# Optimization experiments

Measured on AMD Instinct MI355X. Metric: run time of the kernel, lower is better.

## Reference

```python
import jax, jax.numpy as jnp
import numpy as np

D = 1024
H = 16
HD = D // H
S = 2048
B = 4
EPS = 1e-5


def gelu_tanh(x):
    c = jnp.sqrt(2.0 / jnp.pi).astype(x.dtype)
    return 0.5 * x * (1.0 + jnp.tanh(c * (x + 0.044715 * x ** 3)))


def layernorm(x, gamma, beta):
    mu = jnp.mean(x, axis=-1, keepdims=True)
    var = jnp.var(x, axis=-1, keepdims=True)
    return (x - mu) * jax.lax.rsqrt(var + EPS) * gamma + beta


def setup_inputs() -> dict:
    key = jax.random.key(0)
    ks = jax.random.split(key, 12)
    s = 0.02
    return {
        "x": jax.random.normal(ks[0], (B, S, D), jnp.float32),
        "Wq": jax.random.normal(ks[1], (D, D), jnp.float32) * s,
        "Wk": jax.random.normal(ks[2], (D, D), jnp.float32) * s,
        "Wv": jax.random.normal(ks[3], (D, D), jnp.float32) * s,
        "Wo": jax.random.normal(ks[4], (D, D), jnp.float32) * s,
        "bo": jnp.zeros((D,), jnp.float32),
        "W1": jax.random.normal(ks[5], (D, 4 * D), jnp.float32) * s,
        "b1": jnp.zeros((4 * D,), jnp.float32),
        "W2": jax.random.normal(ks[6], (4 * D, D), jnp.float32) * s,
        "b2": jnp.zeros((D,), jnp.float32),
        "g1": jnp.ones((D,), jnp.float32),
        "be1": jnp.zeros((D,), jnp.float32),
        "g2": jnp.ones((D,), jnp.float32),
        "be2": jnp.zeros((D,), jnp.float32),
    }


def reference(x, Wq, Wk, Wv, Wo, bo, W1, b1, W2, b2, g1, be1, g2, be2):
    b, n, d = x.shape
    # --- attention sub-block (pre-LN) ---
    h = layernorm(x, g1, be1)
    q = (h @ Wq).reshape(b, n, H, HD).transpose(0, 2, 1, 3)  # [b,H,n,hd]
    k = (h @ Wk).reshape(b, n, H, HD).transpose(0, 2, 1, 3)
    v = (h @ Wv).reshape(b, n, H, HD).transpose(0, 2, 1, 3)
    scores = jnp.einsum('bhqd,bhkd->bhqk', q, k) / jnp.sqrt(jnp.float32(HD))
    causal = jnp.tril(jnp.ones((n, n), dtype=bool))
    scores = jnp.where(causal, scores, -jnp.inf)
    w = jax.nn.softmax(scores, axis=-1)  # dropout rate 0 -> identity
    attn = jnp.einsum('bhqk,bhkd->bhqd', w, v)
    attn = attn.transpose(0, 2, 1, 3).reshape(b, n, d)
    x = x + (attn @ Wo + bo)
    # --- FFN sub-block (pre-LN) ---
    h = layernorm(x, g2, be2)
    h = gelu_tanh(h @ W1 + b1) @ W2 + b2
    return x + h
```

## Files before the change

### kernel.cpp

```cpp
#include <hip/hip_runtime.h>
#include <hip/hip_bf16.h>
#include <math.h>


typedef __attribute__((ext_vector_type(8))) short bf16x8;
typedef __attribute__((ext_vector_type(4))) float f32x4;

#define AS1 __attribute__((address_space(1)))
#define AS3 __attribute__((address_space(3)))

__device__ __forceinline__ void gl_lds16(const void* g, void* l) {
  __builtin_amdgcn_global_load_lds((const AS1 void*)g, (AS3 void*)l, 16, 0, 0);
}

__device__ __forceinline__ float gelu_f(float x) {
  const float c = 0.7978845608028654f;
  return 0.5f * x * (1.0f + tanhf(c * (x + 0.044715f * x * x * x)));
}

__device__ __forceinline__ float bf2f(short s) {
  unsigned u = ((unsigned)(unsigned short)s) << 16;
  return __builtin_bit_cast(float, u);
}
__device__ __forceinline__ short f2bf(float f) {
  __hip_bfloat16 h = __float2bfloat16(f);
  return __builtin_bit_cast(short, h);
}

__global__ void __launch_bounds__(256) tcvt_kernel(
    const float* __restrict__ W, __hip_bfloat16* __restrict__ WT, int K, int N) {
  __shared__ float t[32][33];
  const int n0 = blockIdx.x * 32, k0 = blockIdx.y * 32;
  const int tx = threadIdx.x, ty0 = threadIdx.y;
#pragma unroll
  for (int i = 0; i < 4; i++) {
    int ty = ty0 + i * 8;
    t[ty][tx] = W[(size_t)(k0 + ty) * N + n0 + tx];
  }
  __syncthreads();
#pragma unroll
  for (int i = 0; i < 4; i++) {
    int ty = ty0 + i * 8;
    WT[(size_t)(n0 + ty) * K + k0 + tx] = __float2bfloat16(t[tx][ty]);
  }
}

__global__ void __launch_bounds__(256) vtr_kernel(
    const __hip_bfloat16* __restrict__ qkv, __hip_bfloat16* __restrict__ vt) {
  __shared__ __hip_bfloat16 t[32][33];
  const int s0 = blockIdx.x * 32;
  const int hd0 = blockIdx.y * 32;
  const int bh = blockIdx.z;
  const int b = bh >> 4, h = bh & 15;
  const int tx = threadIdx.x, ty0 = threadIdx.y;
  const __hip_bfloat16* src =
      qkv + (size_t)(b * 2048 + s0) * 3072 + 2048 + h * 64 + hd0;
#pragma unroll
  for (int i = 0; i < 4; i++) {
    int ty = ty0 + i * 8;
    t[ty][tx] = src[(size_t)ty * 3072 + tx];
  }
  __syncthreads();
  __hip_bfloat16* dst = vt + ((size_t)bh * 64 + hd0) * 2048 + s0;
#pragma unroll
  for (int i = 0; i < 4; i++) {
    int ty = ty0 + i * 8;
    dst[(size_t)ty * 2048 + tx] = t[tx][ty];
  }
}

__global__ void __launch_bounds__(256) ln_kernel(
    const float* __restrict__ x, const float* __restrict__ gma,
    const float* __restrict__ bta, __hip_bfloat16* __restrict__ out) {
  const int row = blockIdx.x;
  const int tid = threadIdx.x;
  const float4 v = ((const float4*)(x + (size_t)row * 1024))[tid];
  float s = v.x + v.y + v.z + v.w;
  float s2 = v.x * v.x + v.y * v.y + v.z * v.z + v.w * v.w;
#pragma unroll
  for (int m = 32; m; m >>= 1) {
    s += __shfl_xor(s, m);
    s2 += __shfl_xor(s2, m);
  }
  __shared__ float red[8];
  const int w = tid >> 6, lane = tid & 63;
  if (lane == 0) { red[w] = s; red[4 + w] = s2; }
  __syncthreads();
  s = red[0] + red[1] + red[2] + red[3];
  s2 = red[4] + red[5] + red[6] + red[7];
  const float mu = s * (1.0f / 1024.0f);
  const float var = s2 * (1.0f / 1024.0f) - mu * mu;
  const float rs = rsqrtf(var + 1e-5f);
  const float4 gv = ((const float4*)gma)[tid];
  const float4 bv = ((const float4*)bta)[tid];
  __hip_bfloat16* orow = out + (size_t)row * 1024 + tid * 4;
  orow[0] = __float2bfloat16((v.x - mu) * rs * gv.x + bv.x);
  orow[1] = __float2bfloat16((v.y - mu) * rs * gv.y + bv.y);
  orow[2] = __float2bfloat16((v.z - mu) * rs * gv.z + bv.z);
  orow[3] = __float2bfloat16((v.w - mu) * rs * gv.w + bv.w);
}

template <int BM, int BN, int WM, int WN, int EPI>
__global__ void __launch_bounds__(512, 2) gemmT(
    const __hip_bfloat16* __restrict__ Ap, const __hip_bfloat16* __restrict__ Bp,
    void* __restrict__ outp, const float* __restrict__ bias,
    const float* __restrict__ resid, int N, int K) {
  constexpr int PM = BM / WM, PN = BN / WN;
  constexpr int MR = PM / 16, NR = PN / 16;
  constexpr int UA = BM / 128, UB = BN / 128, U = UA + UB;
  constexpr int KSB = (BM + BN) * 64;
  __shared__ __attribute__((aligned(128))) char smem[2 * 2 * KSB];
  const int tid = threadIdx.x;
  const int lane = tid & 63, w = tid >> 6;
  const int wr = w / WN, wc = w % WN;
  const int cr = lane & 15, g = lane >> 4;

  const int gx = gridDim.x;
  const int nwg = gx * gridDim.y;
  const int orig = blockIdx.y * gx + blockIdx.x;
  const int f = (orig & 7) * (nwg >> 3) + (orig >> 3);
  const int sid = f >> 4, wit = f & 15;
  const int stm = gx >> 2;
  const int bm = (sid % stm) * 4 + (wit & 3);
  const int bn = (sid / stm) * 4 + (wit >> 2);
  const int bmr = bm * BM, bnr = bn * BN;
  const int nkt = K >> 6;

  const int srow = tid >> 2;
  const int sq = ((tid & 3) ^ (((srow >> 3) & 1) << 1)) * 8;
  const int rq = (g ^ (((cr >> 3) & 1) << 1)) * 8;

  auto stage_ks = [&](int tt, int ks) {
    char* base = smem + (tt & 1) * (2 * KSB) + ks * KSB;
#pragma unroll
    for (int ua = 0; ua < UA; ua++)
      gl_lds16(Ap + (size_t)(bmr + ua * 128 + srow) * K + tt * 64 + ks * 32 + sq,
               base + ua * 8192 + w * 1024);
#pragma unroll
    for (int ub = 0; ub < UB; ub++)
      gl_lds16(Bp + (size_t)(bnr + ub * 128 + srow) * K + tt * 64 + ks * 32 + sq,
               base + BM * 64 + ub * 8192 + w * 1024);
  };
  auto vmw = [&]() {
    if constexpr (U == 3)
      asm volatile("s_waitcnt vmcnt(9)" ::: "memory");
    else
      asm volatile("s_waitcnt vmcnt(12)" ::: "memory");
  };

  f32x4 acc[MR][NR];
#pragma unroll
  for (int i = 0; i < MR; i++)
#pragma unroll
    for (int j = 0; j < NR; j++) acc[i][j] = (f32x4){0.f, 0.f, 0.f, 0.f};

  auto compute = [&](int t, int ks) {
    const char* base = smem + (t & 1) * (2 * KSB) + ks * KSB;
    const __hip_bfloat16* pA = (const __hip_bfloat16*)base;
    const __hip_bfloat16* pB = (const __hip_bfloat16*)(base + BM * 64);
    bf16x8 av[MR], bv[NR];
#pragma unroll
    for (int m = 0; m < MR; m++)
      av[m] = *(const bf16x8*)(pA + (wr * PM + m * 16 + cr) * 32 + rq);
#pragma unroll
    for (int n = 0; n < NR; n++)
      bv[n] = *(const bf16x8*)(pB + (wc * PN + n * 16 + cr) * 32 + rq);
    __builtin_amdgcn_s_setprio(1);
#pragma unroll
    for (int m = 0; m < MR; m++)
#pragma unroll
      for (int n = 0; n < NR; n++)
        acc[m][n] =
            __builtin_amdgcn_mfma_f32_16x16x32_bf16(av[m], bv[n], acc[m][n], 0, 0, 0);
    __builtin_amdgcn_s_setprio(0);
  };

  stage_ks(0, 0);
  stage_ks(0, 1);
  stage_ks(1, 0);

  for (int t = 0; t < nkt; ++t) {
    stage_ks(t + 1 < nkt ? t + 1 : t - 1, 1);
    vmw();
    __builtin_amdgcn_s_barrier();
    compute(t, 0);
    __builtin_amdgcn_s_barrier();
    stage_ks(t + 2 < nkt ? t + 2 : t, 0);
    vmw();
    __builtin_amdgcn_s_barrier();
    compute(t, 1);
    __builtin_amdgcn_s_barrier();
  }
  asm volatile("s_waitcnt vmcnt(0)" ::: "memory");

#pragma unroll
  for (int m = 0; m < MR; m++) {
#pragma unroll
    for (int rr = 0; rr < 4; rr++) {
      const int row = bmr + wr * PM + m * 16 + g * 4 + rr;
#pragma unroll
      for (int n = 0; n < NR; n++) {
        const int col = bnr + wc * PN + n * 16 + cr;
        float v = acc[m][n][rr];
        if (EPI == 0) {
          ((__hip_bfloat16*)outp)[(size_t)row * N + col] = __float2bfloat16(v);
        } else if (EPI == 1) {
          v += bias[col] + resid[(size_t)row * N + col];
          ((float*)outp)[(size_t)row * N + col] = v;
        } else {
          v = gelu_f(v + bias[col]);
          ((__hip_bfloat16*)outp)[(size_t)row * N + col] = __float2bfloat16(v);
        }
      }
    }
  }
}

__global__ void __launch_bounds__(256) attn_kernel(
    const __hip_bfloat16* __restrict__ qkv, const __hip_bfloat16* __restrict__ vt,
    __hip_bfloat16* __restrict__ o) {
  __shared__ __hip_bfloat16 sK[2][64 * 64];
  __shared__ __hip_bfloat16 sV[2][64 * 64];
  __shared__ __hip_bfloat16 pl[4][16][64];
  const int tid = threadIdx.x, lane = tid & 63, w = tid >> 6;
  const int bid = blockIdx.x;
  const int bh = (bid & 7) + 8 * ((bid >> 3) & 7);
  const int qt = 15 - (bid >> 6);
  const int b = bh >> 4, h = bh & 15;
  const int cr = lane & 15, g = lane >> 4;
  const int qr0 = qt * 128 + w * 32;
  const float NEG = -1e30f;
  const float SC2 = 0.18033688011112042f;
  const int sw = cr & 7;
  const int sg0 = (g ^ sw) * 8;
  const int sg1 = ((g ^ sw) ^ 4) * 8;
  const int pkey = (cr & 7) << 1;

  bf16x8 aq[2][2];
#pragma unroll
  for (int m = 0; m < 2; m++) {
    const __hip_bfloat16* qp =
        qkv + (size_t)(b * 2048 + qr0 + m * 16 + cr) * 3072 + h * 64 + g * 8;
    bf16x8 q0 = *(const bf16x8*)qp;
    bf16x8 q1 = *(const bf16x8*)(qp + 32);
#pragma unroll
    for (int j = 0; j < 8; j++) {
      aq[m][0][j] = f2bf(bf2f(q0[j]) * SC2);
      aq[m][1][j] = f2bf(bf2f(q1[j]) * SC2);
    }
  }
  const __hip_bfloat16* kbase = qkv + (size_t)(b * 2048) * 3072 + 1024 + h * 64;
  const __hip_bfloat16* vbase = vt + (size_t)bh * 64 * 2048;

  const int l8 = lane >> 3, c8 = lane & 7;
  const int c8s = (c8 ^ l8) * 8;
#define STAGE_TILE(bi, ktile)                                                   \
  {                                                                             \
    _Pragma("unroll") for (int i = 0; i < 2; i++) {                             \
      const int rb = (i * 4 + w) * 8 + l8;                                      \
      gl_lds16(kbase + (size_t)((ktile) * 64 + rb) * 3072 + c8s,                \
               &sK[bi][(i * 4 + w) * 512]);                                     \
      gl_lds16(vbase + (size_t)rb * 2048 + (ktile) * 64 + c8s,                  \
               &sV[bi][(i * 4 + w) * 512]);                                     \
    }                                                                           \
  }

  f32x4 oacc[2][4];
#pragma unroll
  for (int m = 0; m < 2; m++)
#pragma unroll
    for (int i = 0; i < 4; i++) oacc[m][i] = (f32x4){0.f, 0.f, 0.f, 0.f};
  float mrow[2] = {NEG, NEG};
  float lrow[2] = {0.f, 0.f};

  const int nkt = (qt + 1) * 2;
  STAGE_TILE(0, 0);
  asm volatile("s_waitcnt vmcnt(0)" ::: "memory");
  __syncthreads();
  int cur = 0;

  for (int kt = 0; kt < nkt; ++kt) {
    if (kt + 1 < nkt) STAGE_TILE(cur ^ 1, kt + 1);

    if (kt * 64 <= qr0 + 31) {
      f32x4 st[4][2];
      __builtin_amdgcn_s_setprio(1);
#pragma unroll
      for (int kf = 0; kf < 4; kf++) {
        const bf16x8 bk0 = *(const bf16x8*)&sK[cur][(kf * 16 + cr) * 64 + sg0];
        const bf16x8 bk1 = *(const bf16x8*)&sK[cur][(kf * 16 + cr) * 64 + sg1];
#pragma unroll
        for (int mq = 0; mq < 2; mq++) {
          f32x4 z = (f32x4){0.f, 0.f, 0.f, 0.f};
          z = __builtin_amdgcn_mfma_f32_16x16x32_bf16(bk0, aq[mq][0], z, 0, 0, 0);
          z = __builtin_amdgcn_mfma_f32_16x16x32_bf16(bk1, aq[mq][1], z, 0, 0, 0);
          st[kf][mq] = z;
        }
      }
      __builtin_amdgcn_s_setprio(0);
      if (kt * 64 + 63 > qr0) {
#pragma unroll
        for (int kf = 0; kf < 4; kf++)
#pragma unroll
          for (int mq = 0; mq < 2; mq++)
#pragma unroll
            for (int rr = 0; rr < 4; rr++) {
              const int kvcol = kt * 64 + kf * 16 + g * 4 + rr;
              const int qrow = qr0 + mq * 16 + cr;
              if (kvcol > qrow) st[kf][mq][rr] = NEG;
            }
      }
#pragma unroll
      for (int mq = 0; mq < 2; mq++) {
        float pmax = st[0][mq][0];
#pragma unroll
        for (int kf = 0; kf < 4; kf++)
#pragma unroll
          for (int rr = 0; rr < 4; rr++)
            pmax = fmaxf(pmax, st[kf][mq][rr]);
        pmax = fmaxf(pmax, __shfl_xor(pmax, 16));
        pmax = fmaxf(pmax, __shfl_xor(pmax, 32));
        if (__any(pmax > mrow[mq] + 8.0f)) {
          const float mn = fmaxf(mrow[mq], pmax);
          const float scl = exp2f(mrow[mq] - mn);
          mrow[mq] = mn;
          lrow[mq] *= scl;
          float s0 = __shfl(scl, g * 4 + 0);
          float s1 = __shfl(scl, g * 4 + 1);
          float s2 = __shfl(scl, g * 4 + 2);
          float s3 = __shfl(scl, g * 4 + 3);
#pragma unroll
          for (int nf = 0; nf < 4; nf++) {
            f32x4 t = oacc[mq][nf];
            t[0] *= s0; t[1] *= s1; t[2] *= s2; t[3] *= s3;
            oacc[mq][nf] = t;
          }
        }
        float rsum = 0.f;
#pragma unroll
        for (int kf = 0; kf < 4; kf++) {
          short4 pk;
#pragma unroll
          for (int rr = 0; rr < 4; rr++) {
            const float p = exp2f(st[kf][mq][rr] - mrow[mq]);
            rsum += p;
            ((short*)&pk)[rr] = f2bf(p);
          }
          const int slot4 = (kf * 4 + g) ^ pkey;
          *(short4*)&pl[w][cr][slot4 * 4] = pk;
        }
        rsum += __shfl_xor(rsum, 16);
        rsum += __shfl_xor(rsum, 32);
        lrow[mq] += rsum;
        const bf16x8 pa0 = *(const bf16x8*)&pl[w][cr][((2 * g) ^ pkey) * 4];
        const bf16x8 pa1 = *(const bf16x8*)&pl[w][cr][((2 * g + 8) ^ pkey) * 4];
        __builtin_amdgcn_s_setprio(1);
#pragma unroll
        for (int nf = 0; nf < 4; nf++) {
          const bf16x8 bv0 = *(const bf16x8*)&sV[cur][(nf * 16 + cr) * 64 + sg0];
          const bf16x8 bv1 = *(const bf16x8*)&sV[cur][(nf * 16 + cr) * 64 + sg1];
          oacc[mq][nf] = __builtin_amdgcn_mfma_f32_16x16x32_bf16(pa0, bv0, oacc[mq][nf], 0, 0, 0);
          oacc[mq][nf] = __builtin_amdgcn_mfma_f32_16x16x32_bf16(pa1, bv1, oacc[mq][nf], 0, 0, 0);
        }
        __builtin_amdgcn_s_setprio(0);
      }
    }

    if (kt + 1 < nkt) {
      asm volatile("s_waitcnt vmcnt(0)" ::: "memory");
      __syncthreads();
      cur ^= 1;
    }
  }

#pragma unroll
  for (int m = 0; m < 2; m++) {
    float il[4];
#pragma unroll
    for (int rr = 0; rr < 4; rr++)
      il[rr] = 1.0f / __shfl(lrow[m], g * 4 + rr);
#pragma unroll
    for (int nf = 0; nf < 4; nf++)
#pragma unroll
      for (int rr = 0; rr < 4; rr++) {
        const int row = qr0 + m * 16 + g * 4 + rr;
        o[(size_t)(b * 2048 + row) * 1024 + h * 64 + nf * 16 + cr] =
            __float2bfloat16(oacc[m][nf][rr] * il[rr]);
      }
  }
#undef STAGE_TILE
}

extern "C" void kernel_launch(void* const* d_in, const int* in_sizes, int n_in,
                              void* d_out, int out_size, void* d_ws, size_t ws_size,
                              hipStream_t stream) {
  const float* x   = (const float*)d_in[0];
  const float* Wq  = (const float*)d_in[1];
  const float* Wk  = (const float*)d_in[2];
  const float* Wv  = (const float*)d_in[3];
  const float* Wo  = (const float*)d_in[4];
  const float* bo  = (const float*)d_in[5];
  const float* W1  = (const float*)d_in[6];
  const float* b1  = (const float*)d_in[7];
  const float* W2  = (const float*)d_in[8];
  const float* b2  = (const float*)d_in[9];
  const float* g1  = (const float*)d_in[10];
  const float* be1 = (const float*)d_in[11];
  const float* g2  = (const float*)d_in[12];
  const float* be2 = (const float*)d_in[13];

  char* ws = (char*)d_ws;
  const size_t MB = 1024 * 1024;
  __hip_bfloat16* hA    = (__hip_bfloat16*)(ws + 0);
  __hip_bfloat16* attnO = (__hip_bfloat16*)(ws + 0);
  __hip_bfloat16* qkv   = (__hip_bfloat16*)(ws + 16 * MB);
  float*          x2    = (float*)(ws + 16 * MB);
  __hip_bfloat16* h2    = (__hip_bfloat16*)(ws + 48 * MB);
  __hip_bfloat16* vtg   = (__hip_bfloat16*)(ws + 64 * MB);
  __hip_bfloat16* act   = (__hip_bfloat16*)(ws + 64 * MB);
  __hip_bfloat16* WqkvT = (__hip_bfloat16*)(ws + 128 * MB);
  __hip_bfloat16* WoT   = (__hip_bfloat16*)(ws + 134 * MB);
  __hip_bfloat16* W1T   = (__hip_bfloat16*)(ws + 136 * MB);
  __hip_bfloat16* W2T   = (__hip_bfloat16*)(ws + 144 * MB);

  const dim3 tb(32, 8);
  tcvt_kernel<<<dim3(32, 32), tb, 0, stream>>>(Wq, WqkvT, 1024, 1024);
  tcvt_kernel<<<dim3(32, 32), tb, 0, stream>>>(Wk, WqkvT + 1024 * 1024, 1024, 1024);
  tcvt_kernel<<<dim3(32, 32), tb, 0, stream>>>(Wv, WqkvT + 2 * 1024 * 1024, 1024, 1024);
  tcvt_kernel<<<dim3(32, 32), tb, 0, stream>>>(Wo, WoT, 1024, 1024);
  tcvt_kernel<<<dim3(128, 32), tb, 0, stream>>>(W1, W1T, 1024, 4096);
  tcvt_kernel<<<dim3(32, 128), tb, 0, stream>>>(W2, W2T, 4096, 1024);

  ln_kernel<<<8192, 256, 0, stream>>>(x, g1, be1, hA);
  gemmT<128, 256, 2, 4, 0><<<dim3(64, 12), 512, 0, stream>>>(
      hA, WqkvT, qkv, nullptr, nullptr, 3072, 1024);
  vtr_kernel<<<dim3(64, 2, 64), tb, 0, stream>>>(qkv, vtg);
  attn_kernel<<<1024, 256, 0, stream>>>(qkv, vtg, attnO);
  gemmT<128, 256, 2, 4, 1><<<dim3(64, 4), 512, 0, stream>>>(
      attnO, WoT, x2, bo, x, 1024, 1024);
  ln_kernel<<<8192, 256, 0, stream>>>(x2, g2, be2, h2);
  gemmT<256, 256, 2, 4, 2><<<dim3(32, 16), 512, 0, stream>>>(
      h2, W1T, act, b1, nullptr, 4096, 1024);
  gemmT<128, 256, 2, 4, 1><<<dim3(64, 4), 512, 0, stream>>>(
      act, W2T, (float*)d_out, b2, x2, 1024, 4096);
  (void)in_sizes; (void)n_in; (void)out_size; (void)ws_size;
}
```

Before: 400.5 us.

## Restructure GEMM into phased K=64 tiles with interleaved per-phase prefetch

Replaces the split 32-wide K-half double buffering with full 64-wide K tiles in an XOR-swizzled LDS layout. The inner loop now runs in phases over pairs of M-fragments, and each phase issues part of the next tile's global-to-LDS loads (A for t+1, B for t+2) before its MFMAs. B fragments are loaded once per tile and reused across phases. The aim is to spread memory issue across compute and cut barrier and waitcnt overhead, at the cost of more barriers per phase and a more fragile prefetch ordering.

```diff
diff --git a/kernel.cpp b/kernel.cpp
--- a/kernel.cpp
+++ b/kernel.cpp
@@ -100,19 +100,23 @@
   orow[3] = __float2bfloat16((v.w - mu) * rs * gv.w + bv.w);
 }
 
-template <int BM, int BN, int WM, int WN, int EPI>
-__global__ void __launch_bounds__(512, 2) gemmT(
+template <int BM, int BN, int EPI>
+__global__ void __launch_bounds__(512, 2) gemm8(
     const __hip_bfloat16* __restrict__ Ap, const __hip_bfloat16* __restrict__ Bp,
     void* __restrict__ outp, const float* __restrict__ bias,
     const float* __restrict__ resid, int N, int K) {
-  constexpr int PM = BM / WM, PN = BN / WN;
-  constexpr int MR = PM / 16, NR = PN / 16;
-  constexpr int UA = BM / 128, UB = BN / 128, U = UA + UB;
-  constexpr int KSB = (BM + BN) * 64;
-  __shared__ __attribute__((aligned(128))) char smem[2 * 2 * KSB];
+  constexpr int PM = BM / 2;
+  constexpr int MR = PM / 16;
+  constexpr int NPH = MR / 2;
+  constexpr int HA = BM / 128;
+  constexpr int ABYTES = BM * 128;
+  constexpr int BBYTES = BN * 128;
+  constexpr int BUFB = ABYTES + BBYTES;
+  __shared__ __attribute__((aligned(128))) char smem[2 * BUFB];
+
   const int tid = threadIdx.x;
   const int lane = tid & 63, w = tid >> 6;
-  const int wr = w / WN, wc = w % WN;
+  const int wr = w >> 2, wc = w & 3;
   const int cr = lane & 15, g = lane >> 4;
 
   const int gx = gridDim.x;
@@ -126,69 +130,92 @@
   const int bmr = bm * BM, bnr = bn * BN;
   const int nkt = K >> 6;
 
-  const int srow = tid >> 2;
-  const int sq = ((tid & 3) ^ (((srow >> 3) & 1) << 1)) * 8;
-  const int rq = (g ^ (((cr >> 3) & 1) << 1)) * 8;
-
-  auto stage_ks = [&](int tt, int ks) {
-    char* base = smem + (tt & 1) * (2 * KSB) + ks * KSB;
-#pragma unroll
-    for (int ua = 0; ua < UA; ua++)
-      gl_lds16(Ap + (size_t)(bmr + ua * 128 + srow) * K + tt * 64 + ks * 32 + sq,
-               base + ua * 8192 + w * 1024);
-#pragma unroll
-    for (int ub = 0; ub < UB; ub++)
-      gl_lds16(Bp + (size_t)(bnr + ub * 128 + srow) * K + tt * 64 + ks * 32 + sq,
-               base + BM * 64 + ub * 8192 + w * 1024);
+  const int srow8 = lane >> 3;
+  const int ssl = ((lane & 7) ^ srow8) * 8;
+  const int rk = cr & 7;
+
+  auto stageA = [&](int tt, int h) {
+    char* base = smem + (tt & 1) * BUFB + h * 16384;
+#pragma unroll
+    for (int c = 0; c < 2; c++) {
+      const int chunk = w + c * 8;
+      gl_lds16(Ap + (size_t)(bmr + h * 128 + chunk * 8 + srow8) * K + tt * 64 + ssl,
+               base + chunk * 1024);
+    }
   };
-  auto vmw = [&]() {
-    if constexpr (U == 3)
-      asm volatile("s_waitcnt vmcnt(9)" ::: "memory");
-    else
-      asm volatile("s_waitcnt vmcnt(12)" ::: "memory");
+  auto stageB = [&](int tt, int h) {
+    char* base = smem + (tt & 1) * BUFB + ABYTES + h * 16384;
+#pragma unroll
+    for (int c = 0; c < 2; c++) {
+      const int chunk = w + c * 8;
+      gl_lds16(Bp + (size_t)(bnr + h * 128 + chunk * 8 + srow8) * K + tt * 64 + ssl,
+               base + chunk * 1024);
+    }
   };
 
-  f32x4 acc[MR][NR];
+  f32x4 acc[MR][4];
 #pragma unroll
   for (int i = 0; i < MR; i++)
 #pragma unroll
-    for (int j = 0; j < NR; j++) acc[i][j] = (f32x4){0.f, 0.f, 0.f, 0.f};
-
-  auto compute = [&](int t, int ks) {
-    const char* base = smem + (t & 1) * (2 * KSB) + ks * KSB;
-    const __hip_bfloat16* pA = (const __hip_bfloat16*)base;
-    const __hip_bfloat16* pB = (const __hip_bfloat16*)(base + BM * 64);
-    bf16x8 av[MR], bv[NR];
-#pragma unroll
-    for (int m = 0; m < MR; m++)
-      av[m] = *(const bf16x8*)(pA + (wr * PM + m * 16 + cr) * 32 + rq);
-#pragma unroll
-    for (int n = 0; n < NR; n++)
-      bv[n] = *(const bf16x8*)(pB + (wc * PN + n * 16 + cr) * 32 + rq);
-    __builtin_amdgcn_s_setprio(1);
-#pragma unroll
-    for (int m = 0; m < MR; m++)
-#pragma unroll
-      for (int n = 0; n < NR; n++)
-        acc[m][n] =
-            __builtin_amdgcn_mfma_f32_16x16x32_bf16(av[m], bv[n], acc[m][n], 0, 0, 0);
-    __builtin_amdgcn_s_setprio(0);
-  };
-
-  stage_ks(0, 0);
-  stage_ks(0, 1);
-  stage_ks(1, 0);
+    for (int j = 0; j < 4; j++) acc[i][j] = (f32x4){0.f, 0.f, 0.f, 0.f};
+  bf16x8 bv[4][2];
+
+#pragma unroll
+  for (int h = 0; h < HA; h++) stageA(0, h);
+  stageB(0, 0); stageB(0, 1);
+  stageB(1, 0); stageB(1, 1);
+  asm volatile("s_waitcnt vmcnt(4)" ::: "memory");
+  __builtin_amdgcn_s_barrier();
 
   for (int t = 0; t < nkt; ++t) {
-    stage_ks(t + 1 < nkt ? t + 1 : t - 1, 1);
-    vmw();
-    __builtin_amdgcn_s_barrier();
-    compute(t, 0);
-    __builtin_amdgcn_s_barrier();
-    stage_ks(t + 2 < nkt ? t + 2 : t, 0);
-    vmw();
-    __builtin_amdgcn_s_barrier();
-    compute(t, 1);
+    const char* buf = smem + (t & 1) * BUFB;
+    const __hip_bfloat16* pA = (const __hip_bfloat16*)buf;
+    const __hip_bfloat16* pB = (const __hip_bfloat16*)(buf + ABYTES);
+    const int tnA = (t + 1 < nkt) ? t + 1 : t - 1;
+    const int tnB = (t + 2 < nkt) ? t + 2 : t;
+#pragma unroll
+    for (int q = 0; q < NPH; q++) {
+      bf16x8 av[2][2];
+#pragma unroll
+      for (int mm = 0; mm < 2; mm++) {
+        const int row = wr * PM + (q * 2 + mm) * 16 + cr;
+#pragma unroll
+        for (int ks = 0; ks < 2; ks++)
+          av[mm][ks] = *(const bf16x8*)(pA + row * 64 + ((ks * 4 + g) ^ rk) * 8);
+      }
+      if (q == 0) {
+#pragma unroll
+        for (int n = 0; n < 4; n++) {
+          const int row = wc * 64 + n * 16 + cr;
+#pragma unroll
+          for (int ks = 0; ks < 2; ks++)
+            bv[n][ks] = *(const bf16x8*)(pB + row * 64 + ((ks * 4 + g) ^ rk) * 8);
+        }
+      }
+      if (NPH == 4) {
+        if (q == 0) stageA(tnA, 0);
+        else if (q == 1) stageA(tnA, 1);
+        else if (q == 2) stageB(tnB, 0);
+        else stageB(tnB, 1);
+      } else {
+        if (q == 0) stageA(tnA, 0);
+        else { stageB(tnB, 0); stageB(tnB, 1); }
+      }
+      __builtin_amdgcn_s_barrier();
+      asm volatile("s_waitcnt lgkmcnt(0)" ::: "memory");
+      __builtin_amdgcn_s_setprio(1);
+#pragma unroll
+      for (int mm = 0; mm < 2; mm++)
+#pragma unroll
+        for (int n = 0; n < 4; n++)
+#pragma unroll
+          for (int ks = 0; ks < 2; ks++)
+            acc[q * 2 + mm][n] = __builtin_amdgcn_mfma_f32_16x16x32_bf16(
+                av[mm][ks], bv[n][ks], acc[q * 2 + mm][n], 0, 0, 0);
+      __builtin_amdgcn_s_setprio(0);
+      __builtin_amdgcn_s_barrier();
+    }
+    asm volatile("s_waitcnt vmcnt(4)" ::: "memory");
     __builtin_amdgcn_s_barrier();
   }
   asm volatile("s_waitcnt vmcnt(0)" ::: "memory");
@@ -199,8 +226,8 @@
     for (int rr = 0; rr < 4; rr++) {
       const int row = bmr + wr * PM + m * 16 + g * 4 + rr;
 #pragma unroll
-      for (int n = 0; n < NR; n++) {
-        const int col = bnr + wc * PN + n * 16 + cr;
+      for (int n = 0; n < 4; n++) {
+        const int col = bnr + wc * 64 + n * 16 + cr;
         float v = acc[m][n][rr];
         if (EPI == 0) {
           ((__hip_bfloat16*)outp)[(size_t)row * N + col] = __float2bfloat16(v);
@@ -432,16 +459,16 @@
   tcvt_kernel<<<dim3(32, 128), tb, 0, stream>>>(W2, W2T, 4096, 1024);
 
   ln_kernel<<<8192, 256, 0, stream>>>(x, g1, be1, hA);
-  gemmT<128, 256, 2, 4, 0><<<dim3(64, 12), 512, 0, stream>>>(
+  gemm8<128, 256, 0><<<dim3(64, 12), 512, 0, stream>>>(
       hA, WqkvT, qkv, nullptr, nullptr, 3072, 1024);
   vtr_kernel<<<dim3(64, 2, 64), tb, 0, stream>>>(qkv, vtg);
   attn_kernel<<<1024, 256, 0, stream>>>(qkv, vtg, attnO);
-  gemmT<128, 256, 2, 4, 1><<<dim3(64, 4), 512, 0, stream>>>(
+  gemm8<128, 256, 1><<<dim3(64, 4), 512, 0, stream>>>(
       attnO, WoT, x2, bo, x, 1024, 1024);
   ln_kernel<<<8192, 256, 0, stream>>>(x2, g2, be2, h2);
-  gemmT<256, 256, 2, 4, 2><<<dim3(32, 16), 512, 0, stream>>>(
+  gemm8<256, 256, 2><<<dim3(32, 16), 512, 0, stream>>>(
       h2, W1T, act, b1, nullptr, 4096, 1024);
-  gemmT<128, 256, 2, 4, 1><<<dim3(64, 4), 512, 0, stream>>>(
+  gemm8<128, 256, 1><<<dim3(64, 4), 512, 0, stream>>>(
       act, W2T, (float*)d_out, b2, x2, 1024, 4096);
   (void)in_sizes; (void)n_in; (void)out_size; (void)ws_size;
 }
```

After: 397.5 us. About the same (-0.8%).
